# Kernel optimization log

Hardware: AMD Instinct MI355X
Metric: run time of the kernel (lower is better)

Reference implementation:

```python
import jax, jax.numpy as jnp
import numpy as np
import math
from jax import lax

IN_C = 512
OUT_C = 512
K = 3
GROUPS = 1
EXP_NITER = 5
MAXC = max(IN_C, OUT_C)
PAD_A = int(math.ceil((K - 1) / 2))  # left/top pad
PAD_B = int(math.floor((K - 1) / 2))  # right/bottom pad


def pad_fct(x):
    # ConstantPad2d((ceil, floor, ceil, floor), 0) on last two dims
    return jnp.pad(x, ((0, 0), (0, 0), (PAD_A, PAD_B), (PAD_A, PAD_B)))


def fast_matrix_conv(m1, m2, groups=1):
    # m1: (m, n, k1, k2); m2: (nb, m//groups, l1, l2)
    # composes two conv kernels: result (nb, n, k+l-1, k+l-1)
    m, n, k1, k2 = m1.shape
    nb, mb, l1, l2 = m2.shape
    x = jnp.transpose(m1, (1, 0, 2, 3))          # (n, m, k1, k2) -> batch=n, chan=m
    w = jnp.flip(m2, (-2, -1))                   # true convolution via flip
    r = lax.conv_general_dilated(
        x, w, window_strides=(1, 1),
        padding=[(l1 - 1, l1 - 1), (l2 - 1, l2 - 1)],
        dimension_numbers=("NCHW", "OIHW", "NCHW"),
        feature_group_count=groups,
    )                                            # (n, nb, k1+l1-1, k2+l2-1)
    return jnp.transpose(r, (1, 0, 2, 3))


def identity_kernel():
    gic = MAXC // GROUPS
    eye = jnp.eye(gic, dtype=jnp.float32)[:, :, None, None]     # (gic, gic, 1, 1)
    eye = jnp.tile(eye[None], (GROUPS, 1, 1, 1, 1)).reshape(MAXC, gic, 1, 1)
    return pad_fct(eye)                                          # (MAXC, gic, K, K)


def setup_inputs() -> dict:
    key = jax.random.key(0)
    kernel = jax.random.normal(key, (MAXC, MAXC // GROUPS, K, K), dtype=jnp.float32) * 0.05
    return {"kernel": kernel}


def reference(kernel):
    kg = kernel + identity_kernel()
    ki = kernel
    for i in range(2, EXP_NITER + 1):
        ki = fast_matrix_conv(ki, kernel, GROUPS) / float(i)
        kg = pad_fct(kg) + ki
    g = GROUPS
    kh, kw = kg.shape[-2], kg.shape[-1]
    kg = kg.reshape(g, MAXC // g, MAXC // g, kh, kw)
    kg = kg[:, : OUT_C // g, : IN_C // g, :, :]
    return kg.reshape(OUT_C, IN_C // g, kh, kw)
```

## Files before the change

kernel.cpp:

```cpp
#include <hip/hip_runtime.h>
#include <stdint.h>

#define C 512
#define C2 262144

typedef __attribute__((ext_vector_type(8))) short bf16x8;
typedef __attribute__((ext_vector_type(4))) float f32x4;

__device__ __forceinline__ unsigned short f2bf(float f) {
    union { float f; uint32_t u; } v; v.f = f;
    uint32_t u = v.u;
    u += 0x7fffu + ((u >> 16) & 1u);
    return (unsigned short)(u >> 16);
}
__device__ __forceinline__ float bf2f(unsigned short h) {
    union { uint32_t u; float f; } v; v.u = ((uint32_t)h) << 16;
    return v.f;
}

#define GL2LDS16(g, l) __builtin_amdgcn_global_load_lds( \
    (const __attribute__((address_space(1))) void*)(g),  \
    (__attribute__((address_space(3))) void*)(l), 16, 0, 0)

__device__ __forceinline__ bf16x8 ldsr16(const char* p) {
    bf16x8 r;
    asm volatile("ds_read_b128 %0, %1"
                 : "=v"(r)
                 : "v"((__attribute__((address_space(3))) const void*)p));
    return r;
}

__device__ __forceinline__ int nth_valid(int mask, int n) {
    int pq = 0;
    while (true) {
        if (mask & 1) { if (n == 0) return pq; --n; }
        mask >>= 1; ++pq;
    }
}

__global__ void k_transform(const float* __restrict__ K,
                            unsigned short* __restrict__ Kt,
                            unsigned short* __restrict__ KtT,
                            float* __restrict__ Ktf) {
    int t = blockIdx.x * 256 + threadIdx.x;
    int a = t >> 9, b = t & 511;
#pragma unroll
    for (int j = 0; j < 9; ++j) {
        float v = K[(size_t)t * 9 + j];
        unsigned short h = f2bf(v);
        Kt[(size_t)j * C2 + t] = h;
        KtT[(size_t)j * C2 + (size_t)b * C + a] = h;
        Ktf[(size_t)j * C2 + (size_t)b * C + a] = v;
    }
}

__global__ void k_sched(int* __restrict__ sched) {
    __shared__ int hist[4][10];
    __shared__ int base[4][10];
    const int tid = threadIdx.x;
    if (tid < 40) ((int*)hist)[tid] = 0;
    if (tid < 4) sched[tid] = 0;
    __syncthreads();
    const int offs[5] = {0, 25, 74, 155, 276};
    int step = -1, yx = 0, V = 0;
    if (tid < 276) {
#pragma unroll
        for (int s = 0; s < 4; ++s)
            if (tid >= offs[s] && tid < offs[s + 1]) { step = s; yx = tid - offs[s]; }
        const int s_out = 5 + 2 * step, s_in = s_out - 2;
        const int y = yx / s_out, x = yx % s_out;
        int vy = 0, vx = 0;
#pragma unroll
        for (int p = 0; p < 3; ++p) {
            if (y - p >= 0 && y - p < s_in) ++vy;
            if (x - p >= 0 && x - p < s_in) ++vx;
        }
        V = vy * vx;
        atomicAdd(&hist[step][V], 1);
    }
    __syncthreads();
    if (tid < 4) {
        int acc = 0;
        for (int v = 9; v >= 1; --v) { base[tid][v] = acc; acc += hist[tid][v]; }
        for (int v = 1; v <= 9; ++v) hist[tid][v] = 0;
    }
    __syncthreads();
    if (tid < 276) {
        const int idx = atomicAdd(&hist[step][V], 1);
        const int slot = base[step][V] + idx;
        int* list = sched + 4 + step * 484;
        list[slot * 4 + 0] = yx * 4 + 0;
        list[slot * 4 + 1] = yx * 4 + 1;
        list[slot * 4 + 2] = yx * 4 + 2;
        list[slot * 4 + 3] = yx * 4 + 3;
    }
}

__global__ __launch_bounds__(512, 2) void k_gemm(
    const unsigned short* __restrict__ A,
    const unsigned short* __restrict__ Bm,
    unsigned short* __restrict__ Out,
    int s_in, int s_out, float alpha,
    int* __restrict__ ctr, const int* __restrict__ list, int n_items)
{
    __shared__ __align__(16) char lds[131072];
    __shared__ int s_item;

    const int tid = threadIdx.x;
    const int lane = tid & 63, wid = tid >> 6;
    const int wr = wid >> 2, wc = wid & 3;
    const int l15 = lane & 15, lhi = lane >> 4;

    const int soff = (tid >> 3) * 1024 + ((((tid & 7) ^ ((tid >> 3) & 7))) << 4);
    const int t16 = tid * 16;

    const int coff0 = ((lhi ^ (l15 & 7)) << 4);
    const int coff1 = (((4 + lhi) ^ (l15 & 7)) << 4);
    const int aoff = wr * 16384 + l15 * 128;
    const int boff = 32768 + wc * 8192 + l15 * 128;

    const char* Abase = (const char*)A;
    const char* Bbase = (const char*)Bm;

#define STAGE4(SRC, DSTOFF) { \
        const char* s_ = (SRC) + soff; \
        GL2LDS16(s_,          lds + (DSTOFF) + t16); \
        GL2LDS16(s_ + 65536,  lds + (DSTOFF) + 8192 + t16); \
        GL2LDS16(s_ + 131072, lds + (DSTOFF) + 16384 + t16); \
        GL2LDS16(s_ + 196608, lds + (DSTOFF) + 24576 + t16); \
    }

    for (;;) {
        __syncthreads();
        if (tid == 0) s_item = atomicAdd(ctr, 1);
        __syncthreads();
        const int itm = s_item;
        if (itm >= n_items) break;
        const int code = list[itm];
        const int yx = code >> 2, quad = code & 3;
        const int i0 = (quad & 1) * 256, o0 = (quad >> 1) * 256;
        const int y = yx / s_out, x = yx % s_out;

        int mask = 0, V = 0;
        for (int pq = 0; pq < 9; ++pq) {
            int u = y - pq / 3, v = x - pq % 3;
            if (u >= 0 && u < s_in && v >= 0 && v < s_in) { mask |= 1 << pq; ++V; }
        }

        auto slabA = [&](int pq) {
            int u = y - pq / 3, v = x - pq % 3;
            return Abase + ((size_t)(u * s_in + v) * C + i0) * (size_t)(C * 2);
        };
        auto slabB = [&](int pq) {
            return Bbase + ((size_t)pq * C + o0) * (size_t)(C * 2);
        };
        const int pq0 = nth_valid(mask, 0);
        const char* slA = slabA(pq0);
        const char* slB = slabB(pq0);
        const char* nsA = slA;
        const char* nsB = slB;
        if (V > 1) { int p1 = nth_valid(mask, 1); nsA = slabA(p1); nsB = slabB(p1); }

        f32x4 acc[8][4] = {};
        bf16x8 bBa[4], bBb[4];
        bf16x8 aE[4], aO[4];

        STAGE4(slA, 0)
        STAGE4(slB, 32768)
        asm volatile("s_waitcnt vmcnt(0)" ::: "memory");
        __builtin_amdgcn_s_barrier();
        __builtin_amdgcn_sched_barrier(0);
#pragma unroll
        for (int n = 0; n < 4; ++n)
            bBa[n] = ldsr16(lds + boff + n * 2048 + coff0);
#pragma unroll
        for (int mi = 0; mi < 4; ++mi)
            aE[mi] = ldsr16(lds + aoff + mi * 2048 + coff0);

        const int NI = 8 * V;
        for (int it = 0; it < NI; ++it) {
            const int itl = it & 7;
            const bool lastq = (itl == 7);
            const bool dummy = lastq && (((it >> 3) + 1) >= V);
            const char* sAe = lastq ? nsA : slA;
            const char* sBe = lastq ? nsB : slB;
            const int kb = lastq ? 0 : (itl + 1) * 128;
            const char* cur = lds + (it & 1) * 65536;
            const char* nxt = lds + ((it & 1) ^ 1) * 65536;

#define PHASE(PH) { \
        constexpr int mh_ = (PH) & 1; \
        constexpr int mhn_ = ((PH) + 1) & 1; \
        constexpr int parn_ = ((PH) == 3) ? 0 : (((PH) + 1) >> 1); \
        const int coffn_ = parn_ ? coff1 : coff0; \
         \
        { \
            const char* ab_ = ((PH) == 3) ? nxt : cur; \
            _Pragma("unroll") for (int mi = 0; mi < 4; ++mi) { \
                bf16x8 t0 = ldsr16(ab_ + aoff + mhn_ * 8192 + mi * 2048 + coffn_); \
                if constexpr (((PH) & 1) == 0) aO[mi] = t0; else aE[mi] = t0; \
            } \
        } \
         \
        if constexpr ((PH) == 1) { \
            _Pragma("unroll") for (int n = 0; n < 4; ++n) \
                bBb[n] = ldsr16(cur + boff + n * 2048 + coff1); \
        } \
        if constexpr ((PH) == 3) { \
            _Pragma("unroll") for (int n = 0; n < 4; ++n) \
                bBa[n] = ldsr16(nxt + boff + n * 2048 + coff0); \
        } \
         \
        if constexpr ((PH) == 0) { if (!dummy) STAGE4(sAe + kb, ((it & 1) ^ 1) * 65536) } \
        if constexpr ((PH) == 1) { if (!dummy) STAGE4(sBe + kb, ((it & 1) ^ 1) * 65536 + 32768) } \
        if constexpr ((PH) == 1 || (PH) == 3) { \
            asm volatile("s_waitcnt lgkmcnt(8)" ::: "memory"); \
        } else { \
            asm volatile("s_waitcnt lgkmcnt(4)" ::: "memory"); \
        } \
        __builtin_amdgcn_sched_barrier(0); \
        __builtin_amdgcn_s_setprio(1); \
        _Pragma("unroll") for (int mi = 0; mi < 4; ++mi) \
        _Pragma("unroll") for (int n = 0; n < 4; ++n) { \
            if constexpr ((PH) == 0) \
                acc[mi][n] = __builtin_amdgcn_mfma_f32_16x16x32_bf16(aE[mi], bBa[n], acc[mi][n], 0, 0, 0); \
            else if constexpr ((PH) == 1) \
                acc[4 + mi][n] = __builtin_amdgcn_mfma_f32_16x16x32_bf16(aO[mi], bBa[n], acc[4 + mi][n], 0, 0, 0); \
            else if constexpr ((PH) == 2) \
                acc[mi][n] = __builtin_amdgcn_mfma_f32_16x16x32_bf16(aE[mi], bBb[n], acc[mi][n], 0, 0, 0); \
            else \
                acc[4 + mi][n] = __builtin_amdgcn_mfma_f32_16x16x32_bf16(aO[mi], bBb[n], acc[4 + mi][n], 0, 0, 0); \
        } \
        __builtin_amdgcn_s_setprio(0); \
        if constexpr ((PH) == 2) { \
            asm volatile("s_waitcnt vmcnt(0)" ::: "memory"); \
            __builtin_amdgcn_s_barrier(); \
            __builtin_amdgcn_sched_barrier(0); \
        } \
        if constexpr ((PH) == 3) { \
            __builtin_amdgcn_s_barrier(); \
            __builtin_amdgcn_sched_barrier(0); \
        } \
    }

            PHASE(0) PHASE(1) PHASE(2) PHASE(3)
#undef PHASE

            if (lastq) {
                slA = nsA; slB = nsB;
                int vn = (it >> 3) + 2;
                if (vn < V) {
                    int pqn = nth_valid(mask, vn);
                    nsA = slabA(pqn); nsB = slabB(pqn);
                }
            }
        }
        asm volatile("s_waitcnt lgkmcnt(0)" ::: "memory");
        __builtin_amdgcn_sched_barrier(0);

#pragma unroll
        for (int M = 0; M < 8; ++M) {
#pragma unroll
            for (int r = 0; r < 4; ++r) {
                const int irow = i0 + wr * 128 + M * 16 + lhi * 4 + r;
                unsigned short* op = Out + ((size_t)yx * C + irow) * C
                                   + o0 + wc * 64 + l15;
#pragma unroll
                for (int n = 0; n < 4; ++n)
                    op[n * 16] = f2bf(acc[M][n][r] * alpha);
            }
        }
    }
#undef STAGE4
    asm volatile("s_waitcnt vmcnt(0)" ::: "memory");
}

__global__ __launch_bounds__(256) void k_final(
    const unsigned short* __restrict__ Ka, int sa, int ofa,
    const unsigned short* __restrict__ Kb, int sb, int ofb,
    const float* __restrict__ Ktf, float* __restrict__ kg, int init)
{
    __shared__ float L[64 * 121];
    const int i = blockIdx.x;
    const int o0 = blockIdx.y * 64;
    const int tid = threadIdx.x, lane = tid & 63, wid = tid >> 6;

    for (int idx = tid; idx < 64 * 121; idx += 256) L[idx] = 0.f;
    __syncthreads();

    const int sa2 = sa * sa;
    for (int yxv = wid; yxv < sa2; yxv += 4) {
        float v = bf2f(Ka[((size_t)yxv * C + i) * C + o0 + lane]);
        int yy = yxv / sa + ofa, xx = yxv % sa + ofa;
        L[lane * 121 + yy * 11 + xx] += v;
    }
    __syncthreads();
    const int sb2 = sb * sb;
    for (int yxv = wid; yxv < sb2; yxv += 4) {
        float v = bf2f(Kb[((size_t)yxv * C + i) * C + o0 + lane]);
        int yy = yxv / sb + ofb, xx = yxv % sb + ofb;
        L[lane * 121 + yy * 11 + xx] += v;
    }
    __syncthreads();
    if (init) {
        for (int j = wid; j < 9; j += 4) {
            float v = Ktf[(size_t)j * C2 + (size_t)i * C + o0 + lane];
            if (j == 4 && (o0 + lane) == i) v += 1.0f;
            L[lane * 121 + (j / 3 + 4) * 11 + (j % 3 + 4)] += v;
        }
    }
    __syncthreads();
    if (init) {
        for (int idx = tid; idx < 64 * 121; idx += 256) {
            int ol = idx / 121, w = idx - ol * 121;
            kg[((size_t)(o0 + ol) * C + i) * 121 + w] = L[idx];
        }
    } else {
        for (int idx = tid; idx < 64 * 121; idx += 256) {
            int ol = idx / 121, w = idx - ol * 121;
            kg[((size_t)(o0 + ol) * C + i) * 121 + w] += L[idx];
        }
    }
}

__global__ __launch_bounds__(256) void k_final4(
    const unsigned short* __restrict__ K2, const unsigned short* __restrict__ K3,
    const unsigned short* __restrict__ K4, const unsigned short* __restrict__ K5,
    const float* __restrict__ Ktf, float* __restrict__ kg)
{
    __shared__ float L[64 * 121];
    const int i = blockIdx.x;
    const int o0 = blockIdx.y * 64;
    const int tid = threadIdx.x, lane = tid & 63, wid = tid >> 6;

    for (int idx = tid; idx < 64 * 121; idx += 256) L[idx] = 0.f;
    __syncthreads();

#define ADDSRC(SRC, S, OFS) { \
        const int s2_ = (S) * (S); \
        for (int yxv = wid; yxv < s2_; yxv += 4) { \
            float v = bf2f((SRC)[((size_t)yxv * C + i) * C + o0 + lane]); \
            int yy = yxv / (S) + (OFS), xx = yxv % (S) + (OFS); \
            L[lane * 121 + yy * 11 + xx] += v; \
        } \
        __syncthreads(); \
    }
    ADDSRC(K2, 5, 3) ADDSRC(K3, 7, 2) ADDSRC(K4, 9, 1) ADDSRC(K5, 11, 0)
#undef ADDSRC

    for (int j = wid; j < 9; j += 4) {
        float v = Ktf[(size_t)j * C2 + (size_t)i * C + o0 + lane];
        if (j == 4 && (o0 + lane) == i) v += 1.0f;
        L[lane * 121 + (j / 3 + 4) * 11 + (j % 3 + 4)] += v;
    }
    __syncthreads();
    for (int idx = tid; idx < 64 * 121; idx += 256) {
        int ol = idx / 121, w = idx - ol * 121;
        kg[((size_t)(o0 + ol) * C + i) * 121 + w] = L[idx];
    }
}

extern "C" void kernel_launch(void* const* d_in, const int* in_sizes, int n_in,
                              void* d_out, int out_size, void* d_ws, size_t ws_size,
                              hipStream_t stream) {
    const float* K = (const float*)d_in[0];
    float* kg = (float*)d_out;
    char* ws = (char*)d_ws;

    unsigned short* Kt  = (unsigned short*)(ws);
    unsigned short* KtT = (unsigned short*)(ws + (size_t)4718592);
    float*          Ktf = (float*)         (ws + (size_t)9437184);

    const bool big = (ws_size >= (size_t)163585616);

    if (big) {
        unsigned short* Ki2 = (unsigned short*)(ws + (size_t)18874368);
        unsigned short* Ki3 = (unsigned short*)(ws + (size_t)31981568);
        unsigned short* Ki4 = (unsigned short*)(ws + (size_t)57671680);
        unsigned short* Ki5 = (unsigned short*)(ws + (size_t)100139008);
        int* sch = (int*)(ws + (size_t)163577856);
        int* ctr = sch;
        int* lst = sch + 4;

        k_transform<<<1024, 256, 0, stream>>>(K, Kt, KtT, Ktf);
        k_sched<<<1, 320, 0, stream>>>(sch);
        k_gemm<<<256, 512, 0, stream>>>(KtT, Kt, Ki2, 3, 5, 0.5f,
                                        ctr + 0, lst + 0 * 484, 100);
        k_gemm<<<256, 512, 0, stream>>>(Ki2, Kt, Ki3, 5, 7, 1.0f / 3.0f,
                                        ctr + 1, lst + 1 * 484, 196);
        k_gemm<<<256, 512, 0, stream>>>(Ki3, Kt, Ki4, 7, 9, 0.25f,
                                        ctr + 2, lst + 2 * 484, 324);
        k_gemm<<<256, 512, 0, stream>>>(Ki4, Kt, Ki5, 9, 11, 0.2f,
                                        ctr + 3, lst + 3 * 484, 484);
        k_final4<<<dim3(512, 8), 256, 0, stream>>>(Ki2, Ki3, Ki4, Ki5, Ktf, kg);
    } else {
        unsigned short* P1 = (unsigned short*)(ws + (size_t)18874368);
        unsigned short* P2 = (unsigned short*)(ws + (size_t)61341696);
        int* sch = (int*)(ws + (size_t)124780544);
        int* ctr = sch;
        int* lst = sch + 4;

        k_transform<<<1024, 256, 0, stream>>>(K, Kt, KtT, Ktf);
        k_sched<<<1, 320, 0, stream>>>(sch);
        k_gemm<<<256, 512, 0, stream>>>(KtT, Kt, P1, 3, 5, 0.5f,
                                        ctr + 0, lst + 0 * 484, 100);
        k_gemm<<<256, 512, 0, stream>>>(P1, Kt, P2, 5, 7, 1.0f / 3.0f,
                                        ctr + 1, lst + 1 * 484, 196);
        k_final<<<dim3(512, 8), 256, 0, stream>>>(P1, 5, 3, P2, 7, 2, Ktf, kg, 1);
        k_gemm<<<256, 512, 0, stream>>>(P2, Kt, P1, 7, 9, 0.25f,
                                        ctr + 2, lst + 2 * 484, 324);
        k_gemm<<<256, 512, 0, stream>>>(P1, Kt, P2, 9, 11, 0.2f,
                                        ctr + 3, lst + 3 * 484, 484);
        k_final<<<dim3(512, 8), 256, 0, stream>>>(P1, 9, 1, P2, 11, 0, Ktf, kg, 0);
    }
}
```

Before: 610.9 us.

## Split long work items along the reduction dimension and merge partial sums

The scheduler now splits output tiles whose tap count is six or more into two halves of the 3x3 reduction in the first three GEMM steps. Each half is its own work item, and the second half writes to a scratch buffer. A new merge kernel then adds the partial result back into the output in bf16. This aims to cut tail imbalance in the persistent GEMM, where too few long items were left for 256 blocks. The cost is extra kernel launches, extra global traffic for the partials, and an additional bf16 rounding on the merged values.

```diff
diff --git a/kernel.cpp b/kernel.cpp
--- a/kernel.cpp
+++ b/kernel.cpp
@@ -54,7 +54,7 @@
     }
 }
 
-__global__ void k_sched(int* __restrict__ sched) {
+__global__ void k_sched(int* __restrict__ sched, int split_mask) {
     __shared__ int hist[4][10];
     __shared__ int base[4][10];
     const int tid = threadIdx.x;
@@ -62,7 +62,8 @@
     if (tid < 4) sched[tid] = 0;
     __syncthreads();
     const int offs[5] = {0, 25, 74, 155, 276};
-    int step = -1, yx = 0, V = 0;
+    const int Loff[4] = {0, 120, 400, 904};
+    int step = -1, yx = 0, cW = 0, cD = 0;
     if (tid < 276) {
 #pragma unroll
         for (int s = 0; s < 4; ++s)
@@ -75,25 +76,56 @@
             if (y - p >= 0 && y - p < s_in) ++vy;
             if (x - p >= 0 && x - p < s_in) ++vx;
         }
-        V = vy * vx;
-        atomicAdd(&hist[step][V], 1);
+        const int V = vy * vx;
+        const bool sp = ((split_mask >> step) & 1) && (V >= 6);
+        cW = sp ? (V + 1) / 2 : V;
+        cD = V - cW;
+        atomicAdd(&hist[step][cW], 1);
+        if (cD > 0) atomicAdd(&hist[step][cD], 1);
     }
     __syncthreads();
     if (tid < 4) {
-        int acc = 0;
-        for (int v = 9; v >= 1; --v) { base[tid][v] = acc; acc += hist[tid][v]; }
-        for (int v = 1; v <= 9; ++v) hist[tid][v] = 0;
+        int a = 0;
+        for (int v = 9; v >= 1; --v) { base[tid][v] = a; a += hist[tid][v]; hist[tid][v] = 0; }
     }
     __syncthreads();
     if (tid < 276) {
-        const int idx = atomicAdd(&hist[step][V], 1);
-        const int slot = base[step][V] + idx;
-        int* list = sched + 4 + step * 484;
-        list[slot * 4 + 0] = yx * 4 + 0;
-        list[slot * 4 + 1] = yx * 4 + 1;
-        list[slot * 4 + 2] = yx * 4 + 2;
-        list[slot * 4 + 3] = yx * 4 + 3;
-    }
+        int* L = sched + 4 + Loff[step];
+        {
+            const int idx = atomicAdd(&hist[step][cW], 1);
+            int* w = L + (base[step][cW] + idx) * 4;
+            w[0] = yx * 8 + 0; w[1] = yx * 8 + 2; w[2] = yx * 8 + 4; w[3] = yx * 8 + 6;
+        }
+        if (cD > 0) {
+            const int idx = atomicAdd(&hist[step][cD], 1);
+            int* d = L + (base[step][cD] + idx) * 4;
+            d[0] = yx * 8 + 1; d[1] = yx * 8 + 3; d[2] = yx * 8 + 5; d[3] = yx * 8 + 7;
+        }
+    }
+}
+
+__global__ __launch_bounds__(256) void k_merge(
+    unsigned short* __restrict__ Out, const unsigned short* __restrict__ P,
+    const int* __restrict__ list)
+{
+    const int code = list[blockIdx.x];
+    if (!(code & 1)) return;
+    const int quad = (code >> 1) & 3, yx = code >> 3;
+    const int i0 = (quad & 1) * 256, o0 = (quad >> 1) * 256;
+    const int t = threadIdx.x;
+    const int r = blockIdx.y * 16 + (t >> 4);
+    const int c = (t & 15) * 16;
+    const size_t base = ((size_t)yx * C + i0 + r) * C + o0 + c;
+    bf16x8* po = (bf16x8*)(Out + base);
+    const bf16x8* pp = (const bf16x8*)(P + base);
+    bf16x8 a0 = po[0], a1 = po[1];
+    bf16x8 b0 = pp[0], b1 = pp[1];
+#pragma unroll
+    for (int k = 0; k < 8; ++k) {
+        a0[k] = (short)f2bf(bf2f((unsigned short)a0[k]) + bf2f((unsigned short)b0[k]));
+        a1[k] = (short)f2bf(bf2f((unsigned short)a1[k]) + bf2f((unsigned short)b1[k]));
+    }
+    po[0] = a0; po[1] = a1;
 }
 
 __global__ __launch_bounds__(512, 2) void k_gemm(
@@ -101,7 +133,8 @@
     const unsigned short* __restrict__ Bm,
     unsigned short* __restrict__ Out,
     int s_in, int s_out, float alpha,
-    int* __restrict__ ctr, const int* __restrict__ list, int n_items)
+    int* __restrict__ ctr, const int* __restrict__ list, int n_items,
+    unsigned short* __restrict__ Pout, int split)
 {
     __shared__ __align__(16) char lds[131072];
     __shared__ int s_item;
@@ -137,7 +170,9 @@
         const int itm = s_item;
         if (itm >= n_items) break;
         const int code = list[itm];
-        const int yx = code >> 2, quad = code & 3;
+        const int isD = code & 1;
+        const int quad = (code >> 1) & 3;
+        const int yx = code >> 3;
         const int i0 = (quad & 1) * 256, o0 = (quad >> 1) * 256;
         const int y = yx / s_out, x = yx % s_out;
 
@@ -146,6 +181,10 @@
             int u = y - pq / 3, v = x - pq % 3;
             if (u >= 0 && u < s_in && v >= 0 && v < s_in) { mask |= 1 << pq; ++V; }
         }
+        const int h = (split && V >= 6) ? (V + 1) / 2 : V;
+        const int c0 = isD ? h : 0;
+        const int cnt = isD ? (V - h) : h;
+        unsigned short* ob = isD ? Pout : Out;
 
         auto slabA = [&](int pq) {
             int u = y - pq / 3, v = x - pq % 3;
@@ -154,12 +193,12 @@
         auto slabB = [&](int pq) {
             return Bbase + ((size_t)pq * C + o0) * (size_t)(C * 2);
         };
-        const int pq0 = nth_valid(mask, 0);
+        const int pq0 = nth_valid(mask, c0);
         const char* slA = slabA(pq0);
         const char* slB = slabB(pq0);
         const char* nsA = slA;
         const char* nsB = slB;
-        if (V > 1) { int p1 = nth_valid(mask, 1); nsA = slabA(p1); nsB = slabB(p1); }
+        if (cnt > 1) { int p1 = nth_valid(mask, c0 + 1); nsA = slabA(p1); nsB = slabB(p1); }
 
         f32x4 acc[8][4] = {};
         bf16x8 bBa[4], bBb[4];
@@ -177,11 +216,11 @@
         for (int mi = 0; mi < 4; ++mi)
             aE[mi] = ldsr16(lds + aoff + mi * 2048 + coff0);
 
-        const int NI = 8 * V;
+        const int NI = 8 * cnt;
         for (int it = 0; it < NI; ++it) {
             const int itl = it & 7;
             const bool lastq = (itl == 7);
-            const bool dummy = lastq && (((it >> 3) + 1) >= V);
+            const bool dummy = lastq && (((it >> 3) + 1) >= cnt);
             const char* sAe = lastq ? nsA : slA;
             const char* sBe = lastq ? nsB : slB;
             const int kb = lastq ? 0 : (itl + 1) * 128;
@@ -249,8 +288,8 @@
             if (lastq) {
                 slA = nsA; slB = nsB;
                 int vn = (it >> 3) + 2;
-                if (vn < V) {
-                    int pqn = nth_valid(mask, vn);
+                if (vn < cnt) {
+                    int pqn = nth_valid(mask, c0 + vn);
                     nsA = slabA(pqn); nsB = slabB(pqn);
                 }
             }
@@ -263,7 +302,7 @@
 #pragma unroll
             for (int r = 0; r < 4; ++r) {
                 const int irow = i0 + wr * 128 + M * 16 + lhi * 4 + r;
-                unsigned short* op = Out + ((size_t)yx * C + irow) * C
+                unsigned short* op = ob + ((size_t)yx * C + irow) * C
                                    + o0 + wc * 64 + l15;
 #pragma unroll
                 for (int n = 0; n < 4; ++n)
@@ -379,38 +418,44 @@
         unsigned short* Ki4 = (unsigned short*)(ws + (size_t)57671680);
         unsigned short* Ki5 = (unsigned short*)(ws + (size_t)100139008);
         int* sch = (int*)(ws + (size_t)163577856);
-        int* ctr = sch;
         int* lst = sch + 4;
+        unsigned short* Pb = Ki5;
 
         k_transform<<<1024, 256, 0, stream>>>(K, Kt, KtT, Ktf);
-        k_sched<<<1, 320, 0, stream>>>(sch);
+        k_sched<<<1, 320, 0, stream>>>(sch, 0x7);
         k_gemm<<<256, 512, 0, stream>>>(KtT, Kt, Ki2, 3, 5, 0.5f,
-                                        ctr + 0, lst + 0 * 484, 100);
+                                        sch + 0, lst + 0, 120, Pb, 1);
+        k_merge<<<dim3(120, 16), 256, 0, stream>>>(Ki2, Pb, lst + 0);
         k_gemm<<<256, 512, 0, stream>>>(Ki2, Kt, Ki3, 5, 7, 1.0f / 3.0f,
-                                        ctr + 1, lst + 1 * 484, 196);
+                                        sch + 1, lst + 120, 280, Pb, 1);
+        k_merge<<<dim3(280, 16), 256, 0, stream>>>(Ki3, Pb, lst + 120);
         k_gemm<<<256, 512, 0, stream>>>(Ki3, Kt, Ki4, 7, 9, 0.25f,
-                                        ctr + 2, lst + 2 * 484, 324);
+                                        sch + 2, lst + 400, 504, Pb, 1);
+        k_merge<<<dim3(504, 16), 256, 0, stream>>>(Ki4, Pb, lst + 400);
         k_gemm<<<256, 512, 0, stream>>>(Ki4, Kt, Ki5, 9, 11, 0.2f,
-                                        ctr + 3, lst + 3 * 484, 484);
+                                        sch + 3, lst + 904, 484, Pb, 0);
         k_final4<<<dim3(512, 8), 256, 0, stream>>>(Ki2, Ki3, Ki4, Ki5, Ktf, kg);
     } else {
         unsigned short* P1 = (unsigned short*)(ws + (size_t)18874368);
         unsigned short* P2 = (unsigned short*)(ws + (size_t)61341696);
         int* sch = (int*)(ws + (size_t)124780544);
-        int* ctr = sch;
         int* lst = sch + 4;
+        unsigned short* Pb2 = P2;
+        unsigned short* Pb3 = P1 + 6553600;
 
         k_transform<<<1024, 256, 0, stream>>>(K, Kt, KtT, Ktf);
-        k_sched<<<1, 320, 0, stream>>>(sch);
+        k_sched<<<1, 320, 0, stream>>>(sch, 0x3);
         k_gemm<<<256, 512, 0, stream>>>(KtT, Kt, P1, 3, 5, 0.5f,
-                                        ctr + 0, lst + 0 * 484, 100);
+                                        sch + 0, lst + 0, 120, Pb2, 1);
+        k_merge<<<dim3(120, 16), 256, 0, stream>>>(P1, Pb2, lst + 0);
         k_gemm<<<256, 512, 0, stream>>>(P1, Kt, P2, 5, 7, 1.0f / 3.0f,
-                                        ctr + 1, lst + 1 * 484, 196);
+                                        sch + 1, lst + 120, 280, Pb3, 1);
+        k_merge<<<dim3(280, 16), 256, 0, stream>>>(P2, Pb3, lst + 120);
         k_final<<<dim3(512, 8), 256, 0, stream>>>(P1, 5, 3, P2, 7, 2, Ktf, kg, 1);
         k_gemm<<<256, 512, 0, stream>>>(P2, Kt, P1, 7, 9, 0.25f,
-                                        ctr + 2, lst + 2 * 484, 324);
+                                        sch + 2, lst + 400, 324, Pb2, 0);
         k_gemm<<<256, 512, 0, stream>>>(P1, Kt, P2, 9, 11, 0.2f,
-                                        ctr + 3, lst + 3 * 484, 484);
+                                        sch + 3, lst + 904, 484, Pb2, 0);
         k_final<<<dim3(512, 8), 256, 0, stream>>>(P1, 9, 1, P2, 11, 0, Ktf, kg, 0);
     }
 }
```

Result: faster. 544.6 us (-10.9%).
